# Performance work log

Measured on AMD Instinct MI355X. Metric: run time of the kernel, lower is better.

## Reference

```python
import jax, jax.numpy as jnp
import numpy as np


def setup_inputs() -> dict:
    key = jax.random.key(0)
    k1, k2, k3 = jax.random.split(key, 3)
    B, Q, K, D = 4, 2048, 2048, 1024
    query = jax.random.normal(k1, (B, Q, D), dtype=jnp.float32)
    value = jax.random.normal(k2, (B, K, D), dtype=jnp.float32)
    attention_mask = jax.random.randint(k3, (B, Q, K), 0, 2, dtype=jnp.int32)
    return {"query": query, "value": value, "attention_mask": attention_mask}


def reference(query, value, attention_mask):
    # key defaults to value in the original module
    D = query.shape[-1]
    # scores[b,q,k] = sum_d (query[b,q,d] + key[b,k,d])
    #              = rowsum(query)[b,q] + rowsum(key)[b,k]  (separable outer-sum,
    # avoids the (B,Q,K,D) intermediate the torch code materializes)
    q_sum = query.sum(-1)                    # (B, Q)
    k_sum = value.sum(-1)                    # (B, K)  (key == value)
    scores = q_sum[:, :, None] + k_sum[:, None, :]   # (B, Q, K)
    scores = scores / jnp.sqrt(jnp.asarray(D, scores.dtype))  # use_scale=True
    mask_value = -1e9
    scores = scores + (1.0 - attention_mask.astype(scores.dtype)) * mask_value
    attention_weights = jax.nn.softmax(scores, axis=-1)       # (B, Q, K)
    context_vector = jnp.einsum('bqk,bkd->bqd', attention_weights, value)
    return (context_vector, attention_weights)
```

## Files before the change

### kernel.cpp

```cpp
#include <hip/hip_runtime.h>
#include <stdint.h>

#define BB 4
#define QQ 2048
#define KK 2048
#define DD 1024

__device__ inline unsigned short f2bf(float f) {
    unsigned int u = __float_as_uint(f);
    unsigned int r = (u + 0x7fffu + ((u >> 16) & 1u)) >> 16;
    return (unsigned short)r;
}

typedef short bf16x8 __attribute__((ext_vector_type(8)));
typedef float f32x4  __attribute__((ext_vector_type(4)));

__device__ inline void async16(const void* g, void* l) {
    __builtin_amdgcn_global_load_lds(
        (const __attribute__((address_space(1))) unsigned int*)g,
        (__attribute__((address_space(3))) unsigned int*)l,
        16, 0, 0);
}

__global__ __launch_bounds__(256) void transpose_sum(const float* __restrict__ V,
                                                     unsigned short* __restrict__ Vt,
                                                     float* __restrict__ s) {
    int bid = blockIdx.x;
    int b  = bid >> 9;
    int r  = bid & 511;
    int kt = r >> 4;
    int dt = r & 15;
    int k0 = kt * 64, d0 = dt * 64;
    __shared__ float tile[64 * 65];
    int t = threadIdx.x;
    for (int i = 0; i < 4; i++) {
        int idx = i * 256 + t;
        int row = idx >> 4;
        int c4  = idx & 15;
        float4 v = *(const float4*)(V + (size_t)(b * KK + k0 + row) * DD + d0 + c4 * 4);
        float* p = &tile[row * 65 + c4 * 4];
        p[0] = v.x; p[1] = v.y; p[2] = v.z; p[3] = v.w;
        float ps = (v.x + v.y) + (v.z + v.w);
        ps += __shfl_xor(ps, 8, 16);
        ps += __shfl_xor(ps, 4, 16);
        ps += __shfl_xor(ps, 2, 16);
        ps += __shfl_xor(ps, 1, 16);
        if (c4 == 0) atomicAdd(s + (size_t)b * KK + k0 + row, ps);
    }
    __syncthreads();
    for (int i = 0; i < 2; i++) {
        int idx = i * 256 + t;
        int dr = idx >> 3;
        int kc = idx & 7;
        union { unsigned short u[8]; int4 v; } o;
        #pragma unroll
        for (int m = 0; m < 8; m++)
            o.u[m] = f2bf(tile[(kc * 8 + m) * 65 + dr]);
        *(int4*)(Vt + (size_t)(b * DD + d0 + dr) * KK + k0 + kc * 8) = o.v;
    }
}

__global__ __launch_bounds__(256) void weights_k(const int* __restrict__ mask,
                                                 const float* __restrict__ s,
                                                 float* __restrict__ wout,
                                                 unsigned short* __restrict__ wb16) {
    int wave = threadIdx.x >> 6, lane = threadIdx.x & 63;
    int row = blockIdx.x * 4 + wave;
    int b = row >> 11;
    const int4*   mp = (const int4*)(mask + (size_t)row * KK);
    const float4* ep = (const float4*)(s + (size_t)b * KK);
    float4 w[8];
    float ss = 0.f;
    for (int j = 0; j < 8; j++) {
        int4   m  = mp[lane + j * 64];
        float4 sv = ep[lane + j * 64];
        float4 ev;
        ev.x = __expf(sv.x * 0.03125f);
        ev.y = __expf(sv.y * 0.03125f);
        ev.z = __expf(sv.z * 0.03125f);
        ev.w = __expf(sv.w * 0.03125f);
        w[j].x = m.x ? ev.x : 0.f;
        w[j].y = m.y ? ev.y : 0.f;
        w[j].z = m.z ? ev.z : 0.f;
        w[j].w = m.w ? ev.w : 0.f;
        ss += (w[j].x + w[j].y) + (w[j].z + w[j].w);
    }
    for (int off = 32; off; off >>= 1) ss += __shfl_xor(ss, off, 64);
    float rS = 1.f / ss;
    float4*  wp = (float4*)(wout + (size_t)row * KK);
    ushort4* bp = (ushort4*)(wb16 + (size_t)row * KK);
    for (int j = 0; j < 8; j++) {
        float4 v = w[j];
        v.x *= rS; v.y *= rS; v.z *= rS; v.w *= rS;
        wp[lane + j * 64] = v;
        ushort4 pk;
        pk.x = f2bf(v.x); pk.y = f2bf(v.y); pk.z = f2bf(v.z); pk.w = f2bf(v.w);
        bp[lane + j * 64] = pk;
    }
}

__global__ __launch_bounds__(512, 4) void gemm_ctx(const unsigned short* __restrict__ Wb,
                                                   const unsigned short* __restrict__ Vt,
                                                   float* __restrict__ ctx) {
    int bid = blockIdx.x;
    int dt = bid >> 6;
    int b  = (bid >> 4) & 3;
    int qt = bid & 15;
    int q0 = qt * 128, n0 = dt * 128;
    __shared__ unsigned short As[2][128 * 64];
    __shared__ unsigned short Bs[3][128 * 64];
    int tid = threadIdx.x, wave = tid >> 6, lane = tid & 63;
    int quad = lane >> 4, lm = lane & 15;
    int wm = wave >> 2;
    int wn = wave & 3;

    int srow   = lane >> 3;
    int schunk = (lane & 7) ^ srow;
    const unsigned short* Ag = Wb + (size_t)(b * QQ + q0 + wave * 16 + srow) * KK + schunk * 8;
    const unsigned short* Bg = Vt + (size_t)(b * DD + n0 + wave * 16 + srow) * KK + schunk * 8;

    int m7 = lm & 7;
    int xa0 = lm * 64 + ((0 + quad) ^ m7) * 8;
    int xa1 = lm * 64 + ((4 + quad) ^ m7) * 8;

    f32x4 acc[4][2];
    for (int i = 0; i < 4; i++)
        for (int j = 0; j < 2; j++) acc[i][j] = 0.f;

#define STAGE_A(buf, kpos) do {                                               \
        unsigned short* d = &As[buf][(wave * 16) * 64];                       \
        for (int c = 0; c < 2; c++)                                           \
            async16(Ag + (size_t)(c * 8) * KK + (kpos), d + c * 8 * 64);      \
    } while (0)

#define STAGE_B(buf, kpos) do {                                               \
        unsigned short* d = &Bs[buf][(wave * 16) * 64];                       \
        for (int c = 0; c < 2; c++)                                           \
            async16(Bg + (size_t)(c * 8) * KK + (kpos), d + c * 8 * 64);      \
    } while (0)

#define COMPUTE(ab, bb) do {                                                  \
        bf16x8 a[4][2], bv[2][2];                                             \
        for (int i = 0; i < 4; i++) {                                         \
            a[i][0] = *(const bf16x8*)&As[ab][(wm * 64 + i * 16) * 64 + xa0]; \
            a[i][1] = *(const bf16x8*)&As[ab][(wm * 64 + i * 16) * 64 + xa1]; \
        }                                                                     \
        for (int j = 0; j < 2; j++) {                                         \
            bv[j][0] = *(const bf16x8*)&Bs[bb][(wn * 32 + j * 16) * 64 + xa0]; \
            bv[j][1] = *(const bf16x8*)&Bs[bb][(wn * 32 + j * 16) * 64 + xa1]; \
        }                                                                     \
        for (int h = 0; h < 2; h++)                                           \
            for (int i = 0; i < 4; i++)                                       \
                for (int j = 0; j < 2; j++)                                   \
                    acc[i][j] = __builtin_amdgcn_mfma_f32_16x16x32_bf16(      \
                        a[i][h], bv[j][h], acc[i][j], 0, 0, 0);               \
    } while (0)

    STAGE_A(0, 0);
    STAGE_B(0, 0);
    STAGE_B(1, 64);
    __builtin_amdgcn_sched_barrier(0);
    asm volatile("s_waitcnt vmcnt(2)" ::: "memory");
    __builtin_amdgcn_s_barrier();

#pragma unroll
    for (int t = 0; t < 32; ++t) {
        if (t + 1 < 32) STAGE_A((t + 1) & 1, (t + 1) * 64);
        if (t + 2 < 32) STAGE_B((t + 2) % 3, (t + 2) * 64);
        COMPUTE(t & 1, t % 3);
        if (t + 1 < 32) {
            __builtin_amdgcn_sched_barrier(0);
            if (t + 2 < 32) {
                asm volatile("s_waitcnt vmcnt(2)" ::: "memory");
            } else {
                asm volatile("s_waitcnt vmcnt(0)" ::: "memory");
            }
            __builtin_amdgcn_sched_barrier(0);
            __builtin_amdgcn_s_barrier();
        }
    }

#undef STAGE_A
#undef STAGE_B
#undef COMPUTE

    for (int i = 0; i < 4; i++) {
        int rowb = q0 + wm * 64 + i * 16 + quad * 4;
        for (int j = 0; j < 2; j++) {
            int col = n0 + wn * 32 + j * 16 + lm;
            for (int rr = 0; rr < 4; rr++)
                ctx[(size_t)(b * QQ + rowb + rr) * DD + col] = acc[i][j][rr];
        }
    }
}

extern "C" void kernel_launch(void* const* d_in, const int* in_sizes, int n_in,
                              void* d_out, int out_size, void* d_ws, size_t ws_size,
                              hipStream_t stream) {
    const float* value = (const float*)d_in[1];
    const int*   mask  = (const int*)d_in[2];
    float* out = (float*)d_out;

    unsigned short* Vt = (unsigned short*)d_ws;
    unsigned short* Wb = Vt + (size_t)BB * DD * KK;
    float* s = (float*)(Wb + (size_t)BB * QQ * KK);

    float* ctx  = out;
    float* wout = out + (size_t)BB * QQ * DD;

    hipMemsetAsync(s, 0, (size_t)BB * KK * sizeof(float), stream);
    transpose_sum<<<BB * 512, 256, 0, stream>>>(value, Vt, s);
    weights_k<<<(BB * QQ) / 4, 256, 0, stream>>>(mask, s, wout, Wb);
    gemm_ctx<<<BB * 128, 512, 0, stream>>>(Wb, Vt, ctx);
}
```

Measured before the change: 240.5 us.

## Enlarge GEMM tile to 256x128 with triple-buffered interleaved prefetch

The context GEMM now uses a 256x128 output tile per block (half as many blocks), triple-buffers both A and B in LDS, and splits each k-step into four phases. Each phase interleaves async global-to-LDS loads with MFMA groups, using per-phase barriers and raised scheduling priority around the MFMAs. The goal is better data reuse per loaded byte and more overlap of memory and compute. In exchange it uses more LDS and accumulator registers, lowers occupancy to 2 blocks per CU, leaves only 256 blocks on the GPU, and adds extra barriers per k-step.

Measured after the change: 250.9 us. 4.3% more time.

```diff
diff --git a/kernel.cpp b/kernel.cpp
--- a/kernel.cpp
+++ b/kernel.cpp
@@ -99,16 +99,16 @@
     }
 }
 
-__global__ __launch_bounds__(512, 4) void gemm_ctx(const unsigned short* __restrict__ Wb,
+__global__ __launch_bounds__(512, 2) void gemm_ctx(const unsigned short* __restrict__ Wb,
                                                    const unsigned short* __restrict__ Vt,
                                                    float* __restrict__ ctx) {
+    __shared__ unsigned short As[3][256 * 64];
+    __shared__ unsigned short Bs[3][128 * 64];
     int bid = blockIdx.x;
-    int dt = bid >> 6;
-    int b  = (bid >> 4) & 3;
-    int qt = bid & 15;
-    int q0 = qt * 128, n0 = dt * 128;
-    __shared__ unsigned short As[2][128 * 64];
-    __shared__ unsigned short Bs[3][128 * 64];
+    int dt = bid >> 5;
+    int b  = (bid >> 3) & 3;
+    int qt = bid & 7;
+    int q0 = qt * 256, n0 = dt * 128;
     int tid = threadIdx.x, wave = tid >> 6, lane = tid & 63;
     int quad = lane >> 4, lm = lane & 15;
     int wm = wave >> 2;
@@ -116,76 +116,92 @@
 
     int srow   = lane >> 3;
     int schunk = (lane & 7) ^ srow;
-    const unsigned short* Ag = Wb + (size_t)(b * QQ + q0 + wave * 16 + srow) * KK + schunk * 8;
-    const unsigned short* Bg = Vt + (size_t)(b * DD + n0 + wave * 16 + srow) * KK + schunk * 8;
+    const unsigned short* Ag = Wb + (size_t)(b * QQ + q0 + wave * 8 + srow) * KK + schunk * 8;
+    const unsigned short* Bg = Vt + (size_t)(b * DD + n0 + wave * 8 + srow) * KK + schunk * 8;
 
     int m7 = lm & 7;
     int xa0 = lm * 64 + ((0 + quad) ^ m7) * 8;
     int xa1 = lm * 64 + ((4 + quad) ^ m7) * 8;
 
-    f32x4 acc[4][2];
-    for (int i = 0; i < 4; i++)
+    f32x4 acc[8][2];
+    for (int i = 0; i < 8; i++)
         for (int j = 0; j < 2; j++) acc[i][j] = 0.f;
 
-#define STAGE_A(buf, kpos) do {                                               \
-        unsigned short* d = &As[buf][(wave * 16) * 64];                       \
-        for (int c = 0; c < 2; c++)                                           \
-            async16(Ag + (size_t)(c * 8) * KK + (kpos), d + c * 8 * 64);      \
-    } while (0)
-
-#define STAGE_B(buf, kpos) do {                                               \
-        unsigned short* d = &Bs[buf][(wave * 16) * 64];                       \
-        for (int c = 0; c < 2; c++)                                           \
-            async16(Bg + (size_t)(c * 8) * KK + (kpos), d + c * 8 * 64);      \
-    } while (0)
-
-#define COMPUTE(ab, bb) do {                                                  \
-        bf16x8 a[4][2], bv[2][2];                                             \
-        for (int i = 0; i < 4; i++) {                                         \
-            a[i][0] = *(const bf16x8*)&As[ab][(wm * 64 + i * 16) * 64 + xa0]; \
-            a[i][1] = *(const bf16x8*)&As[ab][(wm * 64 + i * 16) * 64 + xa1]; \
-        }                                                                     \
-        for (int j = 0; j < 2; j++) {                                         \
-            bv[j][0] = *(const bf16x8*)&Bs[bb][(wn * 32 + j * 16) * 64 + xa0]; \
-            bv[j][1] = *(const bf16x8*)&Bs[bb][(wn * 32 + j * 16) * 64 + xa1]; \
-        }                                                                     \
-        for (int h = 0; h < 2; h++)                                           \
-            for (int i = 0; i < 4; i++)                                       \
-                for (int j = 0; j < 2; j++)                                   \
-                    acc[i][j] = __builtin_amdgcn_mfma_f32_16x16x32_bf16(      \
-                        a[i][h], bv[j][h], acc[i][j], 0, 0, 0);               \
-    } while (0)
-
-    STAGE_A(0, 0);
-    STAGE_B(0, 0);
-    STAGE_B(1, 64);
+#define STAGE_A1(buf, kpos, c) \
+        async16(Ag + (size_t)((c) * 64) * KK + (kpos), \
+                &As[buf][((c) * 64 + wave * 8) * 64])
+#define STAGE_B1(buf, kpos, c) \
+        async16(Bg + (size_t)((c) * 64) * KK + (kpos), \
+                &Bs[buf][((c) * 64 + wave * 8) * 64])
+
+    STAGE_A1(0, 0, 0); STAGE_A1(0, 0, 1); STAGE_A1(0, 0, 2); STAGE_A1(0, 0, 3);
+    STAGE_B1(0, 0, 0); STAGE_B1(0, 0, 1);
+    STAGE_A1(1, 64, 0); STAGE_A1(1, 64, 1); STAGE_A1(1, 64, 2); STAGE_A1(1, 64, 3);
+    STAGE_B1(1, 64, 0); STAGE_B1(1, 64, 1);
     __builtin_amdgcn_sched_barrier(0);
-    asm volatile("s_waitcnt vmcnt(2)" ::: "memory");
+    asm volatile("s_waitcnt vmcnt(6)" ::: "memory");
+    __builtin_amdgcn_sched_barrier(0);
     __builtin_amdgcn_s_barrier();
 
-#pragma unroll
+    int ct = 0;
     for (int t = 0; t < 32; ++t) {
-        if (t + 1 < 32) STAGE_A((t + 1) & 1, (t + 1) * 64);
-        if (t + 2 < 32) STAGE_B((t + 2) % 3, (t + 2) * 64);
-        COMPUTE(t & 1, t % 3);
-        if (t + 1 < 32) {
+        int cs = ct + 2; if (cs >= 3) cs -= 3;
+        int kp = (t + 2) * 64;
+        const unsigned short* Ac = &As[ct][0];
+        const unsigned short* Bc = &Bs[ct][0];
+        bool more = (t + 2 < 32);
+        bf16x8 bv[2][2];
+#pragma unroll
+        for (int p = 0; p < 4; ++p) {
+            if (p == 0) {
+                bv[0][0] = *(const bf16x8*)&Bc[(wn * 32 + 0 * 16) * 64 + xa0];
+                bv[0][1] = *(const bf16x8*)&Bc[(wn * 32 + 0 * 16) * 64 + xa1];
+                bv[1][0] = *(const bf16x8*)&Bc[(wn * 32 + 1 * 16) * 64 + xa0];
+                bv[1][1] = *(const bf16x8*)&Bc[(wn * 32 + 1 * 16) * 64 + xa1];
+            }
+            bf16x8 a[2][2];
+            a[0][0] = *(const bf16x8*)&Ac[(wm * 128 + (2 * p + 0) * 16) * 64 + xa0];
+            a[0][1] = *(const bf16x8*)&Ac[(wm * 128 + (2 * p + 0) * 16) * 64 + xa1];
+            a[1][0] = *(const bf16x8*)&Ac[(wm * 128 + (2 * p + 1) * 16) * 64 + xa0];
+            a[1][1] = *(const bf16x8*)&Ac[(wm * 128 + (2 * p + 1) * 16) * 64 + xa1];
+            if (more) {
+                if (p == 0) { STAGE_A1(cs, kp, 0); STAGE_A1(cs, kp, 1); }
+                if (p == 1) { STAGE_A1(cs, kp, 2); STAGE_A1(cs, kp, 3); }
+                if (p == 2) { STAGE_B1(cs, kp, 0); }
+                if (p == 3) { STAGE_B1(cs, kp, 1); }
+            }
+            __builtin_amdgcn_s_barrier();
+            asm volatile("s_waitcnt lgkmcnt(0)" ::: "memory");
             __builtin_amdgcn_sched_barrier(0);
-            if (t + 2 < 32) {
-                asm volatile("s_waitcnt vmcnt(2)" ::: "memory");
-            } else {
-                asm volatile("s_waitcnt vmcnt(0)" ::: "memory");
+            __builtin_amdgcn_s_setprio(1);
+#pragma unroll
+            for (int h = 0; h < 2; h++)
+#pragma unroll
+                for (int ii = 0; ii < 2; ii++)
+#pragma unroll
+                    for (int j = 0; j < 2; j++)
+                        acc[2 * p + ii][j] = __builtin_amdgcn_mfma_f32_16x16x32_bf16(
+                            a[ii][h], bv[j][h], acc[2 * p + ii][j], 0, 0, 0);
+            __builtin_amdgcn_s_setprio(0);
+            if (p == 3) {
+                __builtin_amdgcn_sched_barrier(0);
+                if (t < 30) {
+                    asm volatile("s_waitcnt vmcnt(6)" ::: "memory");
+                } else if (t == 30) {
+                    asm volatile("s_waitcnt vmcnt(0)" ::: "memory");
+                }
+                __builtin_amdgcn_sched_barrier(0);
             }
-            __builtin_amdgcn_sched_barrier(0);
             __builtin_amdgcn_s_barrier();
         }
-    }
-
-#undef STAGE_A
-#undef STAGE_B
-#undef COMPUTE
-
-    for (int i = 0; i < 4; i++) {
-        int rowb = q0 + wm * 64 + i * 16 + quad * 4;
+        ct = (ct == 2) ? 0 : ct + 1;
+    }
+
+#undef STAGE_A1
+#undef STAGE_B1
+
+    for (int i = 0; i < 8; i++) {
+        int rowb = q0 + wm * 128 + i * 16 + quad * 4;
         for (int j = 0; j < 2; j++) {
             int col = n0 + wn * 32 + j * 16 + lm;
             for (int rr = 0; rr < 4; rr++)
@@ -211,5 +227,5 @@
     hipMemsetAsync(s, 0, (size_t)BB * KK * sizeof(float), stream);
     transpose_sum<<<BB * 512, 256, 0, stream>>>(value, Vt, s);
     weights_k<<<(BB * QQ) / 4, 256, 0, stream>>>(mask, s, wout, Wb);
-    gemm_ctx<<<BB * 128, 512, 0, stream>>>(Wb, Vt, ctx);
-}
+    gemm_ctx<<<256, 512, 0, stream>>>(Wb, Vt, ctx);
+}
```
